# Kernel tuning notes

Hardware: AMD Instinct MI355X
Metric: run time of the kernel (lower is better)

## Reference

```python
import jax, jax.numpy as jnp
import numpy as np

B, S, D, K = 4, 8192, 1024, 1024
TAU = 1.0  # gumbel-softmax temperature


def setup_inputs() -> dict:
    key = jax.random.key(0)
    k1, k2, k3 = jax.random.split(key, 3)
    embeddings = jax.random.normal(k1, (B, S, D), dtype=jnp.float32)
    codebook = jax.random.normal(k2, (K, D), dtype=jnp.float32) * 0.02
    # uniform noise in (0,1) for Gumbel sampling, same shape as logits [B,S,K]
    uniform_noise = jax.random.uniform(k3, (B, S, K), dtype=jnp.float32,
                                       minval=1e-6, maxval=1.0 - 1e-6)
    return {"embeddings": embeddings, "codebook": codebook,
            "uniform_noise": uniform_noise}


def reference(embeddings, codebook, uniform_noise):
    x2 = jnp.sum(embeddings * embeddings, axis=-1, keepdims=True)   # [B,S,1]
    c2 = jnp.sum(codebook * codebook, axis=-1)                      # [K]
    xc = jnp.einsum('bsd,kd->bsk', embeddings, codebook)            # [B,S,K]
    d2 = jnp.maximum(x2 + c2 - 2.0 * xc, 0.0)
    logits = -jnp.sqrt(d2)                                          # [B,S,K]
    # Gumbel-softmax (training path, hard=False)
    gumbel = -jnp.log(-jnp.log(uniform_noise))
    weights = jax.nn.softmax((logits + gumbel) / TAU, axis=-1)      # [B,S,K]
    quantized = jnp.einsum('bsk,kd->bsd', weights, codebook)        # [B,S,D]
    return quantized, logits
```

## Files before the change

kernel.cpp:

```cpp
#include <hip/hip_runtime.h>
#include <hip/hip_bf16.h>

constexpr int MM   = 32768;
constexpr int NN   = 1024;
constexpr int KRED = 1024;
constexpr int LDAB = KRED * 2;

using s16x8 = __attribute__((ext_vector_type(8))) short;
using f32x4 = __attribute__((ext_vector_type(4))) float;

__device__ __forceinline__ unsigned short f2bf(float f) {
  unsigned u = __float_as_uint(f);
  return (unsigned short)((u + 0x7fffu + ((u >> 16) & 1u)) >> 16);
}

__device__ __forceinline__ void gload_lds16(const void* g, void* l) {
  __builtin_amdgcn_global_load_lds(
      (const __attribute__((address_space(1))) void*)g,
      (__attribute__((address_space(3))) void*)l, 16, 0, 0);
}

__device__ __forceinline__ float wave_sum(float v) {
#pragma unroll
  for (int o = 32; o > 0; o >>= 1) v += __shfl_xor(v, o);
  return v;
}

__global__ __launch_bounds__(256) void prep_cb(const float* __restrict__ C,
                                               unsigned short* __restrict__ CB,
                                               unsigned short* __restrict__ CT,
                                               float* __restrict__ c2) {
  int k = blockIdx.x;
  int t = threadIdx.x;
  const float4 v = *(const float4*)(C + (size_t)k * 1024 + t * 4);
  ushort4 b = make_ushort4(f2bf(v.x), f2bf(v.y), f2bf(v.z), f2bf(v.w));
  *(ushort4*)(CB + (size_t)k * 1024 + t * 4) = b;
  CT[(size_t)(t * 4 + 0) * 1024 + k] = b.x;
  CT[(size_t)(t * 4 + 1) * 1024 + k] = b.y;
  CT[(size_t)(t * 4 + 2) * 1024 + k] = b.z;
  CT[(size_t)(t * 4 + 3) * 1024 + k] = b.w;
  float p = v.x * v.x + v.y * v.y + v.z * v.z + v.w * v.w;
  p = wave_sum(p);
  __shared__ float red[4];
  if ((t & 63) == 0) red[t >> 6] = p;
  __syncthreads();
  if (t == 0) c2[k] = red[0] + red[1] + red[2] + red[3];
}

__global__ __launch_bounds__(512) void prep_x(const float* __restrict__ X,
                                              unsigned short* __restrict__ Xb,
                                              float* __restrict__ x2) {
  int tid = threadIdx.x;
  int l = tid & 63, w = tid >> 6;
  int m = blockIdx.x * 8 + w;
  size_t base = (size_t)m * 1024 + l * 4;
  float p = 0.0f;
#pragma unroll
  for (int j = 0; j < 4; ++j) {
    const float4 v = *(const float4*)(X + base + j * 256);
    *(ushort4*)(Xb + base + j * 256) =
        make_ushort4(f2bf(v.x), f2bf(v.y), f2bf(v.z), f2bf(v.w));
    p += v.x * v.x + v.y * v.y + v.z * v.z + v.w * v.w;
  }
  p = wave_sum(p);
  if (l == 0) x2[m] = p;
}

__global__ __launch_bounds__(512) void softmax_k(const float* __restrict__ logits,
                                                 const float* __restrict__ noise,
                                                 unsigned short* __restrict__ W) {
  int tid = threadIdx.x;
  int l = tid & 63, w = tid >> 6;
  int m = blockIdx.x * 8 + w;
  size_t base = (size_t)m * 1024 + l * 4;

  float p[16];
  float ps = 0.0f;
#pragma unroll
  for (int j = 0; j < 4; ++j) {
    const float4 lv = *(const float4*)(logits + base + j * 256);
    const float4 nv = *(const float4*)(noise + base + j * 256);
    p[j * 4 + 0] = __expf(lv.x) * (1.0f / (-__logf(nv.x)));
    p[j * 4 + 1] = __expf(lv.y) * (1.0f / (-__logf(nv.y)));
    p[j * 4 + 2] = __expf(lv.z) * (1.0f / (-__logf(nv.z)));
    p[j * 4 + 3] = __expf(lv.w) * (1.0f / (-__logf(nv.w)));
    ps += p[j * 4 + 0] + p[j * 4 + 1] + p[j * 4 + 2] + p[j * 4 + 3];
  }
  ps = wave_sum(ps);
  float inv = 1.0f / ps;

#pragma unroll
  for (int j = 0; j < 4; ++j) {
    *(ushort4*)(W + base + j * 256) =
        make_ushort4(f2bf(p[j * 4 + 0] * inv), f2bf(p[j * 4 + 1] * inv),
                     f2bf(p[j * 4 + 2] * inv), f2bf(p[j * 4 + 3] * inv));
  }
}

template <int MODE>
__global__ __launch_bounds__(512, 2) void gemm256(const unsigned short* __restrict__ A,
                                                  const unsigned short* __restrict__ Bt,
                                                  float* __restrict__ out,
                                                  const float* __restrict__ x2,
                                                  const float* __restrict__ c2) {
  extern __shared__ char smem[];

  int bid = blockIdx.x;
  int swz = (bid & 7) * 64 + (bid >> 3);
  int bm = swz >> 2, bn = swz & 3;
  int brow0 = bm * 256, bcol0 = bn * 256;

  int tid = threadIdx.x;
  int l = tid & 63, w = tid >> 6;
  int wm = w >> 2, wn = w & 3;
  int lr = l & 15, lh = l >> 4;
  const int xsw = (lr & 7) << 4;

  const char* AbH[2] = { (const char*)A + (size_t)brow0 * LDAB,
                         (const char*)A + (size_t)(brow0 + 128) * LDAB };
  const char* BbH[2] = { (const char*)Bt + (size_t)bcol0 * LDAB,
                         (const char*)Bt + (size_t)(bcol0 + 128) * LDAB };

  const int sr0 = tid >> 3;
  const int sc  = (tid & 7) * 16;
  const int scx0 = sc ^ ((sr0 & 7) << 4);

#define STAGE(gbase, kbyte, ldsreg)                                            \
  do {                                                                         \
    gload_lds16((gbase) + (size_t)sr0 * LDAB + (kbyte) + scx0,                 \
                (ldsreg) + tid * 16);                                          \
    gload_lds16((gbase) + (size_t)(sr0 + 64) * LDAB + (kbyte) + scx0,          \
                (ldsreg) + 8192 + tid * 16);                                   \
  } while (0)

  STAGE(AbH[0], 0, smem + 0);
  STAGE(AbH[1], 0, smem + 16384);
  STAGE(BbH[0], 0, smem + 32768);
  STAGE(BbH[1], 0, smem + 49152);
  STAGE(BbH[0], 128, smem + 65536 + 32768);
  STAGE(BbH[1], 128, smem + 65536 + 49152);
  asm volatile("s_waitcnt vmcnt(4)" ::: "memory");
  __builtin_amdgcn_s_barrier();

  const int aoff0 = wm * 16384 + lr * 128;
  const int boff0 = (wn >> 1) * 16384 + (wn & 1) * 8192 + lr * 128;

  f32x4 acc[8][4] = {};
  s16x8 af[4][2], bf[4][2];

#pragma unroll 2
  for (int t = 0; t < 16; ++t) {
    int p = t & 1;
    char* As  = smem + p * 65536;
    char* Bs  = smem + p * 65536 + 32768;
    char* Asn = smem + (1 - p) * 65536;

#pragma unroll
    for (int mi = 0; mi < 4; ++mi)
#pragma unroll
      for (int ks = 0; ks < 2; ++ks)
        af[mi][ks] = *(const s16x8*)(As + aoff0 + mi * 2048 + ((ks * 64 + lh * 16) ^ xsw));
#pragma unroll
    for (int ni = 0; ni < 2; ++ni)
#pragma unroll
      for (int ks = 0; ks < 2; ++ks)
        bf[ni][ks] = *(const s16x8*)(Bs + boff0 + ni * 2048 + ((ks * 64 + lh * 16) ^ xsw));
    if (t + 1 < 16) STAGE(AbH[0], (t + 1) * 128, Asn + 0);
    __builtin_amdgcn_s_barrier();
    asm volatile("s_waitcnt lgkmcnt(0)" ::: "memory");
    __builtin_amdgcn_sched_barrier(0);
    __builtin_amdgcn_s_setprio(1);
#pragma unroll
    for (int mi = 0; mi < 4; ++mi)
#pragma unroll
      for (int ni = 0; ni < 2; ++ni)
#pragma unroll
        for (int ks = 0; ks < 2; ++ks)
          acc[mi][ni] = __builtin_amdgcn_mfma_f32_16x16x32_bf16(af[mi][ks], bf[ni][ks], acc[mi][ni], 0, 0, 0);
    __builtin_amdgcn_s_setprio(0);
    __builtin_amdgcn_s_barrier();

#pragma unroll
    for (int ni = 0; ni < 2; ++ni)
#pragma unroll
      for (int ks = 0; ks < 2; ++ks)
        bf[2 + ni][ks] = *(const s16x8*)(Bs + boff0 + (2 + ni) * 2048 + ((ks * 64 + lh * 16) ^ xsw));
    if (t + 1 < 16) STAGE(AbH[1], (t + 1) * 128, Asn + 16384);
    __builtin_amdgcn_s_barrier();
    asm volatile("s_waitcnt lgkmcnt(0)" ::: "memory");
    __builtin_amdgcn_sched_barrier(0);
    __builtin_amdgcn_s_setprio(1);
#pragma unroll
    for (int mi = 0; mi < 4; ++mi)
#pragma unroll
      for (int ni = 0; ni < 2; ++ni)
#pragma unroll
        for (int ks = 0; ks < 2; ++ks)
          acc[mi][2 + ni] = __builtin_amdgcn_mfma_f32_16x16x32_bf16(af[mi][ks], bf[2 + ni][ks], acc[mi][2 + ni], 0, 0, 0);
    __builtin_amdgcn_s_setprio(0);
    __builtin_amdgcn_s_barrier();

#pragma unroll
    for (int mi = 0; mi < 4; ++mi)
#pragma unroll
      for (int ks = 0; ks < 2; ++ks)
        af[mi][ks] = *(const s16x8*)(As + aoff0 + (4 + mi) * 2048 + ((ks * 64 + lh * 16) ^ xsw));
    if (t + 2 < 16) STAGE(BbH[0], (t + 2) * 128, Bs + 0);
    __builtin_amdgcn_s_barrier();
    asm volatile("s_waitcnt lgkmcnt(0)" ::: "memory");
    __builtin_amdgcn_sched_barrier(0);
    __builtin_amdgcn_s_setprio(1);
#pragma unroll
    for (int mi = 0; mi < 4; ++mi)
#pragma unroll
      for (int ni = 0; ni < 2; ++ni)
#pragma unroll
        for (int ks = 0; ks < 2; ++ks)
          acc[4 + mi][ni] = __builtin_amdgcn_mfma_f32_16x16x32_bf16(af[mi][ks], bf[ni][ks], acc[4 + mi][ni], 0, 0, 0);
    __builtin_amdgcn_s_setprio(0);
    __builtin_amdgcn_s_barrier();

    if (t + 2 < 16) STAGE(BbH[1], (t + 2) * 128, Bs + 16384);
    __builtin_amdgcn_s_setprio(1);
#pragma unroll
    for (int mi = 0; mi < 4; ++mi)
#pragma unroll
      for (int ni = 0; ni < 2; ++ni)
#pragma unroll
        for (int ks = 0; ks < 2; ++ks)
          acc[4 + mi][2 + ni] = __builtin_amdgcn_mfma_f32_16x16x32_bf16(af[mi][ks], bf[2 + ni][ks], acc[4 + mi][2 + ni], 0, 0, 0);
    __builtin_amdgcn_s_setprio(0);
    __builtin_amdgcn_sched_barrier(0);
    if (t < 14) { asm volatile("s_waitcnt vmcnt(4)" ::: "memory"); }
    else        { asm volatile("s_waitcnt vmcnt(0)" ::: "memory"); }
    __builtin_amdgcn_s_barrier();
  }
#undef STAGE

#pragma unroll
  for (int mi = 0; mi < 8; ++mi) {
    int row0 = brow0 + wm * 128 + mi * 16 + lh * 4;
#pragma unroll
    for (int r = 0; r < 4; ++r) {
      int row = row0 + r;
      float xv = (MODE == 1) ? x2[row] : 0.0f;
#pragma unroll
      for (int ni = 0; ni < 4; ++ni) {
        int col = bcol0 + wn * 64 + ni * 16 + lr;
        float v = acc[mi][ni][r];
        if (MODE == 1) {
          float d2 = xv + c2[col] - 2.0f * v;
          v = -sqrtf(fmaxf(d2, 0.0f));
        }
        out[(size_t)row * NN + col] = v;
      }
    }
  }
}

extern "C" void kernel_launch(void* const* d_in, const int* in_sizes, int n_in,
                              void* d_out, int out_size, void* d_ws, size_t ws_size,
                              hipStream_t stream) {
  const float* emb   = (const float*)d_in[0];
  const float* cb    = (const float*)d_in[1];
  const float* noise = (const float*)d_in[2];

  float* quant  = (float*)d_out;
  float* logits = (float*)d_out + (size_t)MM * NN;

  char* ws = (char*)d_ws;
  unsigned short* XW = (unsigned short*)ws;
  unsigned short* CB = (unsigned short*)(ws + 67108864);
  unsigned short* CT = (unsigned short*)(ws + 69206016);
  float* x2 = (float*)(ws + 71303168);
  float* c2 = (float*)(ws + 71434240);

  static bool attr_done = false;
  if (!attr_done) {
    hipFuncSetAttribute((const void*)gemm256<1>,
                        hipFuncAttributeMaxDynamicSharedMemorySize, 131072);
    hipFuncSetAttribute((const void*)gemm256<0>,
                        hipFuncAttributeMaxDynamicSharedMemorySize, 131072);
    attr_done = true;
  }

  prep_cb<<<dim3(1024), dim3(256), 0, stream>>>(cb, CB, CT, c2);
  prep_x<<<dim3(MM / 8), dim3(512), 0, stream>>>(emb, XW, x2);
  gemm256<1><<<dim3(512), dim3(512), 131072, stream>>>(XW, CB, logits, x2, c2);
  softmax_k<<<dim3(MM / 8), dim3(512), 0, stream>>>(logits, noise, XW);
  gemm256<0><<<dim3(512), dim3(512), 131072, stream>>>(XW, CT, quant, nullptr, nullptr);
}
```

Baseline: 258.0 us.

## Replace 256x256 GEMM tiles with simpler 128x128 double-buffered kernel

Both GEMMs move from a 256x256 tile with 512 threads, 128KB of dynamic LDS and a finely interleaved four-phase pipeline to a 128x128 tile with 256 threads and 64KB of static LDS. The new kernel simply double-buffers whole K-slices, with one barrier and one full vmcnt wait per iteration. The aim is more blocks (2048) for better CU occupancy and less scheduling complexity. In exchange, each tile reuses its loads over fewer outputs, global/L2 traffic rises, and load latency is overlapped less tightly.

```diff
diff --git a/kernel.cpp b/kernel.cpp
--- a/kernel.cpp
+++ b/kernel.cpp
@@ -98,148 +98,81 @@
 }
 
 template <int MODE>
-__global__ __launch_bounds__(512, 2) void gemm256(const unsigned short* __restrict__ A,
+__global__ __launch_bounds__(256, 2) void gemm128(const unsigned short* __restrict__ A,
                                                   const unsigned short* __restrict__ Bt,
                                                   float* __restrict__ out,
                                                   const float* __restrict__ x2,
                                                   const float* __restrict__ c2) {
-  extern __shared__ char smem[];
+  __shared__ __align__(16) char smem[65536];
 
   int bid = blockIdx.x;
-  int swz = (bid & 7) * 64 + (bid >> 3);
-  int bm = swz >> 2, bn = swz & 3;
-  int brow0 = bm * 256, bcol0 = bn * 256;
+  int swz = (bid & 7) * 256 + (bid >> 3);
+  int bm = swz >> 3, bn = swz & 7;
+  int brow0 = bm * 128, bcol0 = bn * 128;
 
   int tid = threadIdx.x;
   int l = tid & 63, w = tid >> 6;
-  int wm = w >> 2, wn = w & 3;
+  int wm = w >> 1, wn = w & 1;
   int lr = l & 15, lh = l >> 4;
   const int xsw = (lr & 7) << 4;
 
-  const char* AbH[2] = { (const char*)A + (size_t)brow0 * LDAB,
-                         (const char*)A + (size_t)(brow0 + 128) * LDAB };
-  const char* BbH[2] = { (const char*)Bt + (size_t)bcol0 * LDAB,
-                         (const char*)Bt + (size_t)(bcol0 + 128) * LDAB };
-
-  const int sr0 = tid >> 3;
-  const int sc  = (tid & 7) * 16;
-  const int scx0 = sc ^ ((sr0 & 7) << 4);
-
-#define STAGE(gbase, kbyte, ldsreg)                                            \
+  const char* Ab = (const char*)A + (size_t)brow0 * LDAB;
+  const char* Bb = (const char*)Bt + (size_t)bcol0 * LDAB;
+
+  const int srow = tid >> 3;
+  const int scx  = ((tid & 7) * 16) ^ ((srow & 7) << 4);
+
+#define STAGE(buf, kbyte)                                                      \
   do {                                                                         \
-    gload_lds16((gbase) + (size_t)sr0 * LDAB + (kbyte) + scx0,                 \
-                (ldsreg) + tid * 16);                                          \
-    gload_lds16((gbase) + (size_t)(sr0 + 64) * LDAB + (kbyte) + scx0,          \
-                (ldsreg) + 8192 + tid * 16);                                   \
+    _Pragma("unroll")                                                          \
+    for (int i = 0; i < 4; ++i) {                                              \
+      gload_lds16(Ab + (size_t)(i * 32 + srow) * LDAB + (kbyte) + scx,         \
+                  smem + (buf) * 32768 + i * 4096 + tid * 16);                 \
+      gload_lds16(Bb + (size_t)(i * 32 + srow) * LDAB + (kbyte) + scx,         \
+                  smem + (buf) * 32768 + 16384 + i * 4096 + tid * 16);         \
+    }                                                                          \
   } while (0)
 
-  STAGE(AbH[0], 0, smem + 0);
-  STAGE(AbH[1], 0, smem + 16384);
-  STAGE(BbH[0], 0, smem + 32768);
-  STAGE(BbH[1], 0, smem + 49152);
-  STAGE(BbH[0], 128, smem + 65536 + 32768);
-  STAGE(BbH[1], 128, smem + 65536 + 49152);
-  asm volatile("s_waitcnt vmcnt(4)" ::: "memory");
+  STAGE(0, 0);
+  asm volatile("s_waitcnt vmcnt(0)" ::: "memory");
   __builtin_amdgcn_s_barrier();
 
-  const int aoff0 = wm * 16384 + lr * 128;
-  const int boff0 = (wn >> 1) * 16384 + (wn & 1) * 8192 + lr * 128;
-
-  f32x4 acc[8][4] = {};
-  s16x8 af[4][2], bf[4][2];
-
-#pragma unroll 2
+  const int aoff = wm * 8192 + lr * 128;
+  const int boff = wn * 8192 + lr * 128;
+
+  f32x4 acc[4][4] = {};
+
   for (int t = 0; t < 16; ++t) {
     int p = t & 1;
-    char* As  = smem + p * 65536;
-    char* Bs  = smem + p * 65536 + 32768;
-    char* Asn = smem + (1 - p) * 65536;
-
+    const char* As = smem + p * 32768;
+    const char* Bs = smem + p * 32768 + 16384;
+
+    if (t + 1 < 16) STAGE(1 - p, (t + 1) * 128);
+
+    s16x8 af[4][2], bf[4][2];
 #pragma unroll
     for (int mi = 0; mi < 4; ++mi)
 #pragma unroll
-      for (int ks = 0; ks < 2; ++ks)
-        af[mi][ks] = *(const s16x8*)(As + aoff0 + mi * 2048 + ((ks * 64 + lh * 16) ^ xsw));
-#pragma unroll
-    for (int ni = 0; ni < 2; ++ni)
-#pragma unroll
-      for (int ks = 0; ks < 2; ++ks)
-        bf[ni][ks] = *(const s16x8*)(Bs + boff0 + ni * 2048 + ((ks * 64 + lh * 16) ^ xsw));
-    if (t + 1 < 16) STAGE(AbH[0], (t + 1) * 128, Asn + 0);
-    __builtin_amdgcn_s_barrier();
-    asm volatile("s_waitcnt lgkmcnt(0)" ::: "memory");
-    __builtin_amdgcn_sched_barrier(0);
-    __builtin_amdgcn_s_setprio(1);
+      for (int ks = 0; ks < 2; ++ks) {
+        af[mi][ks] = *(const s16x8*)(As + aoff + mi * 2048 + ((ks * 64 + lh * 16) ^ xsw));
+        bf[mi][ks] = *(const s16x8*)(Bs + boff + mi * 2048 + ((ks * 64 + lh * 16) ^ xsw));
+      }
 #pragma unroll
     for (int mi = 0; mi < 4; ++mi)
 #pragma unroll
-      for (int ni = 0; ni < 2; ++ni)
+      for (int ni = 0; ni < 4; ++ni)
 #pragma unroll
         for (int ks = 0; ks < 2; ++ks)
           acc[mi][ni] = __builtin_amdgcn_mfma_f32_16x16x32_bf16(af[mi][ks], bf[ni][ks], acc[mi][ni], 0, 0, 0);
-    __builtin_amdgcn_s_setprio(0);
+
+    asm volatile("s_waitcnt vmcnt(0)" ::: "memory");
     __builtin_amdgcn_s_barrier();
-
-#pragma unroll
-    for (int ni = 0; ni < 2; ++ni)
-#pragma unroll
-      for (int ks = 0; ks < 2; ++ks)
-        bf[2 + ni][ks] = *(const s16x8*)(Bs + boff0 + (2 + ni) * 2048 + ((ks * 64 + lh * 16) ^ xsw));
-    if (t + 1 < 16) STAGE(AbH[1], (t + 1) * 128, Asn + 16384);
-    __builtin_amdgcn_s_barrier();
-    asm volatile("s_waitcnt lgkmcnt(0)" ::: "memory");
-    __builtin_amdgcn_sched_barrier(0);
-    __builtin_amdgcn_s_setprio(1);
-#pragma unroll
-    for (int mi = 0; mi < 4; ++mi)
-#pragma unroll
-      for (int ni = 0; ni < 2; ++ni)
-#pragma unroll
-        for (int ks = 0; ks < 2; ++ks)
-          acc[mi][2 + ni] = __builtin_amdgcn_mfma_f32_16x16x32_bf16(af[mi][ks], bf[2 + ni][ks], acc[mi][2 + ni], 0, 0, 0);
-    __builtin_amdgcn_s_setprio(0);
-    __builtin_amdgcn_s_barrier();
-
-#pragma unroll
-    for (int mi = 0; mi < 4; ++mi)
-#pragma unroll
-      for (int ks = 0; ks < 2; ++ks)
-        af[mi][ks] = *(const s16x8*)(As + aoff0 + (4 + mi) * 2048 + ((ks * 64 + lh * 16) ^ xsw));
-    if (t + 2 < 16) STAGE(BbH[0], (t + 2) * 128, Bs + 0);
-    __builtin_amdgcn_s_barrier();
-    asm volatile("s_waitcnt lgkmcnt(0)" ::: "memory");
-    __builtin_amdgcn_sched_barrier(0);
-    __builtin_amdgcn_s_setprio(1);
-#pragma unroll
-    for (int mi = 0; mi < 4; ++mi)
-#pragma unroll
-      for (int ni = 0; ni < 2; ++ni)
-#pragma unroll
-        for (int ks = 0; ks < 2; ++ks)
-          acc[4 + mi][ni] = __builtin_amdgcn_mfma_f32_16x16x32_bf16(af[mi][ks], bf[ni][ks], acc[4 + mi][ni], 0, 0, 0);
-    __builtin_amdgcn_s_setprio(0);
-    __builtin_amdgcn_s_barrier();
-
-    if (t + 2 < 16) STAGE(BbH[1], (t + 2) * 128, Bs + 16384);
-    __builtin_amdgcn_s_setprio(1);
-#pragma unroll
-    for (int mi = 0; mi < 4; ++mi)
-#pragma unroll
-      for (int ni = 0; ni < 2; ++ni)
-#pragma unroll
-        for (int ks = 0; ks < 2; ++ks)
-          acc[4 + mi][2 + ni] = __builtin_amdgcn_mfma_f32_16x16x32_bf16(af[mi][ks], bf[2 + ni][ks], acc[4 + mi][2 + ni], 0, 0, 0);
-    __builtin_amdgcn_s_setprio(0);
-    __builtin_amdgcn_sched_barrier(0);
-    if (t < 14) { asm volatile("s_waitcnt vmcnt(4)" ::: "memory"); }
-    else        { asm volatile("s_waitcnt vmcnt(0)" ::: "memory"); }
-    __builtin_amdgcn_s_barrier();
   }
 #undef STAGE
 
 #pragma unroll
-  for (int mi = 0; mi < 8; ++mi) {
-    int row0 = brow0 + wm * 128 + mi * 16 + lh * 4;
+  for (int mi = 0; mi < 4; ++mi) {
+    int row0 = brow0 + wm * 64 + mi * 16 + lh * 4;
 #pragma unroll
     for (int r = 0; r < 4; ++r) {
       int row = row0 + r;
@@ -275,18 +208,9 @@
   float* x2 = (float*)(ws + 71303168);
   float* c2 = (float*)(ws + 71434240);
 
-  static bool attr_done = false;
-  if (!attr_done) {
-    hipFuncSetAttribute((const void*)gemm256<1>,
-                        hipFuncAttributeMaxDynamicSharedMemorySize, 131072);
-    hipFuncSetAttribute((const void*)gemm256<0>,
-                        hipFuncAttributeMaxDynamicSharedMemorySize, 131072);
-    attr_done = true;
-  }
-
   prep_cb<<<dim3(1024), dim3(256), 0, stream>>>(cb, CB, CT, c2);
   prep_x<<<dim3(MM / 8), dim3(512), 0, stream>>>(emb, XW, x2);
-  gemm256<1><<<dim3(512), dim3(512), 131072, stream>>>(XW, CB, logits, x2, c2);
+  gemm128<1><<<dim3(2048), dim3(256), 0, stream>>>(XW, CB, logits, x2, c2);
   softmax_k<<<dim3(MM / 8), dim3(512), 0, stream>>>(logits, noise, XW);
-  gemm256<0><<<dim3(512), dim3(512), 131072, stream>>>(XW, CT, quant, nullptr, nullptr);
-}
+  gemm128<0><<<dim3(2048), dim3(256), 0, stream>>>(XW, CT, quant, nullptr, nullptr);
+}
```

Measured after the change: 280.9 us. +8.9%, slower.
